# Performance work log

Measured on AMD Instinct MI355X. Metric: run time of the kernel, lower is better.

## Reference

```python
import jax, jax.numpy as jnp
import numpy as np

N, C, H, W = 64, 128, 32, 32
EPS = 1e-5


def _layernorm_chw(x, w, b):
    # LayerNorm over normalized_shape=(C,H,W): last 3 dims
    mu = jnp.mean(x, axis=(1, 2, 3), keepdims=True)
    var = jnp.var(x, axis=(1, 2, 3), keepdims=True)
    return (x - mu) * jax.lax.rsqrt(var + EPS) * w[None] + b[None]


def _conv1x1(x, w, b):
    # x: [N,C,H,W], w: [Cout,Cin], b: [Cout]
    return jnp.einsum('oc,nchw->nohw', w, x) + b[None, :, None, None]


def setup_inputs() -> dict:
    key = jax.random.key(0)
    ks = jax.random.split(key, 12)
    d = {
        'query': jax.random.normal(ks[0], (N, C, H, W), jnp.float32),
        'key': jax.random.normal(ks[1], (N, C, H, W), jnp.float32),
        'value': jax.random.normal(ks[2], (N, C, H, W), jnp.float32),
        'ln1_w': jnp.ones((C, H, W), jnp.float32),
        'ln1_b': jnp.zeros((C, H, W), jnp.float32),
        'ln2_w': jnp.ones((C, H, W), jnp.float32),
        'ln2_b': jnp.zeros((C, H, W), jnp.float32),
        'ln3_w': jnp.ones((C, H, W), jnp.float32),
        'ln3_b': jnp.zeros((C, H, W), jnp.float32),
        'wq': jax.random.normal(ks[3], (C, C), jnp.float32) / np.sqrt(C),
        'bq': jnp.zeros((C,), jnp.float32),
        'wk': jax.random.normal(ks[4], (C, C), jnp.float32) / np.sqrt(C),
        'bk': jnp.zeros((C,), jnp.float32),
        'wv': jax.random.normal(ks[5], (C, C), jnp.float32) / np.sqrt(C),
        'bv': jnp.zeros((C,), jnp.float32),
    }
    return d


def reference(query, key, value, ln1_w, ln1_b, ln2_w, ln2_b, ln3_w, ln3_b,
              wq, bq, wk, bk, wv, bv):
    qn = _layernorm_chw(query, ln1_w, ln1_b)  # residual uses normalized query
    kn = _layernorm_chw(key, ln2_w, ln2_b)
    vn = _layernorm_chw(value, ln3_w, ln3_b)
    q = _conv1x1(qn, wq, bq).reshape(N, C, H * W)
    k = _conv1x1(kn, wk, bk).reshape(N, C, H * W)
    v = _conv1x1(vn, wv, bv).reshape(N, C, H * W)
    # attention[n,i,j] = sum_c k[n,c,i] q[n,c,j] / sqrt(C); softmax over i (dim=1)
    attn = jnp.einsum('nci,ncj->nij', k, q) / jnp.sqrt(jnp.float32(C))
    attn = jax.nn.softmax(attn, axis=1)
    out = jnp.einsum('nci,nij->ncj', v, attn).reshape(N, C, H, W)
    x = qn + out
    return x.reshape(N, -1)  # flatten(start_dim=1)
```

## Files before the change

kernel.cpp:

```cpp
#include <hip/hip_runtime.h>


#define NS 64
#define CD 128
#define SD 1024
#define MEL (CD*SD)
#define SCALE2 0.1275174464f

typedef __attribute__((ext_vector_type(4))) float floatx4;
typedef __attribute__((ext_vector_type(8))) short short8;
typedef __attribute__((ext_vector_type(4))) short short4v;

typedef __attribute__((address_space(1))) const void global_cvoid;
typedef __attribute__((address_space(3))) void lds_void;

__device__ __forceinline__ void gl16(const void* g, void* l) {
  __builtin_amdgcn_global_load_lds((global_cvoid*)g, (lds_void*)l, 16, 0, 0);
}
__device__ __forceinline__ unsigned short f2bf(float f) {
  union { float f; unsigned int i; } v; v.f = f;
  unsigned int i = v.i;
  return (unsigned short)((i + 0x7fffu + ((i >> 16) & 1u)) >> 16);
}
__device__ __forceinline__ unsigned int pkbf(float lo, float hi) {
  unsigned int r;
  asm("v_cvt_pk_bf16_f32 %0, %1, %2" : "=v"(r) : "v"(lo), "v"(hi));
  return r;
}
__device__ __forceinline__ float fexp2(float x) {
  float r; asm("v_exp_f32 %0, %1" : "=v"(r) : "v"(x)); return r;
}
__device__ __forceinline__ short8 ld8_bf16(const float* __restrict__ p) {
  floatx4 a = *(const floatx4*)p;
  floatx4 b = *(const floatx4*)(p + 4);
  union { unsigned int u[4]; short8 s; } r;
  r.u[0] = pkbf(a[0], a[1]);
  r.u[1] = pkbf(a[2], a[3]);
  r.u[2] = pkbf(b[0], b[1]);
  r.u[3] = pkbf(b[2], b[3]);
  return r.s;
}
__device__ __forceinline__ floatx4 mfma16(short8 a, short8 b, floatx4 c) {
  return __builtin_amdgcn_mfma_f32_16x16x32_bf16(a, b, c, 0, 0, 0);
}

__global__ __launch_bounds__(512) void stats_kernel(
    const float* __restrict__ q, const float* __restrict__ k,
    const float* __restrict__ v, float* __restrict__ sums)
{
  int b = blockIdx.x;
  int tn = b >> 2, part = b & 3;
  int t = tn >> 6;
  const float* x = (t == 0 ? q : (t == 1 ? k : v))
                 + (size_t)(tn & 63) * MEL + part * (MEL / 4);
  float s1 = 0.f, s2 = 0.f;
#pragma unroll
  for (int it = 0; it < 16; ++it) {
    floatx4 u = *(const floatx4*)(x + it * 2048 + threadIdx.x * 4);
#pragma unroll
    for (int j = 0; j < 4; ++j) { float f = u[j]; s1 += f; s2 += f * f; }
  }
#pragma unroll
  for (int off = 32; off; off >>= 1) {
    s1 += __shfl_xor(s1, off, 64);
    s2 += __shfl_xor(s2, off, 64);
  }
  __shared__ float r1[8], r2[8];
  int w = threadIdx.x >> 6;
  if ((threadIdx.x & 63) == 0) { r1[w] = s1; r2[w] = s2; }
  __syncthreads();
  if (threadIdx.x == 0) {
    float a = 0.f, c = 0.f;
#pragma unroll
    for (int i = 0; i < 8; ++i) { a += r1[i]; c += r2[i]; }
    sums[part * 192 + tn] = a;
    sums[768 + part * 192 + tn] = c;
  }
}

__device__ __forceinline__ void ln_coeffs(const float* __restrict__ sums,
                                          int g, float& a_ln, float& b_ln)
{
  float s1 = ((sums[g] + sums[192 + g]) + (sums[384 + g] + sums[576 + g]));
  float s2 = ((sums[768 + g] + sums[960 + g]) + (sums[1152 + g] + sums[1344 + g]));
  float mu  = s1 * (1.f / MEL);
  float var = s2 * (1.f / MEL) - mu * mu;
  float rs  = rsqrtf(var + 1e-5f);
  a_ln = rs; b_ln = -mu * rs;
}

__global__ __launch_bounds__(512, 4) void proj_kernel(
  const float* __restrict__ k, const float* __restrict__ v,
  const float* __restrict__ l2w, const float* __restrict__ l2b,
  const float* __restrict__ l3w, const float* __restrict__ l3b,
  const float* __restrict__ wk, const float* __restrict__ bk,
  const float* __restrict__ wv, const float* __restrict__ bv,
  const float* __restrict__ sums,
  unsigned short* __restrict__ kT, unsigned short* __restrict__ vN)
{
  int n  = blockIdx.x, t = blockIdx.y, st = blockIdx.z;
  const float* x  = (t == 0 ? k : v) + (size_t)n * MEL;
  const float* lw = (t == 0 ? l2w : l3w);
  const float* lb = (t == 0 ? l2b : l3b);
  const float* W  = (t == 0 ? wk : wv);
  const float* Bs = (t == 0 ? bk : bv);

  float a_ln, b_ln;
  ln_coeffs(sums, (t + 1) * 64 + n, a_ln, b_ln);

  __shared__ __align__(16) unsigned short Xt[128 * 136];

  int tid = threadIdx.x;
  int cb = tid & 15, sb = (tid >> 4) & 15, half = tid >> 8;
  int s0 = st * 128;

  unsigned int w32[8][2];
#pragma unroll
  for (int pr = 0; pr < 2; ++pr) {
    int c0 = cb * 8 + half * 4 + pr * 2;
    const float* xp0 = x  + (size_t)c0 * SD + s0 + sb * 8;
    const float* wp0 = lw + (size_t)c0 * SD + s0 + sb * 8;
    const float* bp0 = lb + (size_t)c0 * SD + s0 + sb * 8;
    float xv0[8], xv1[8], wv0[8], wv1[8], bv0[8], bv1[8];
    *(floatx4*)xv0 = *(const floatx4*)xp0;       *(floatx4*)(xv0+4) = *(const floatx4*)(xp0+4);
    *(floatx4*)xv1 = *(const floatx4*)(xp0+SD);  *(floatx4*)(xv1+4) = *(const floatx4*)(xp0+SD+4);
    *(floatx4*)wv0 = *(const floatx4*)wp0;       *(floatx4*)(wv0+4) = *(const floatx4*)(wp0+4);
    *(floatx4*)wv1 = *(const floatx4*)(wp0+SD);  *(floatx4*)(wv1+4) = *(const floatx4*)(wp0+SD+4);
    *(floatx4*)bv0 = *(const floatx4*)bp0;       *(floatx4*)(bv0+4) = *(const floatx4*)(bp0+4);
    *(floatx4*)bv1 = *(const floatx4*)(bp0+SD);  *(floatx4*)(bv1+4) = *(const floatx4*)(bp0+SD+4);
#pragma unroll
    for (int js = 0; js < 8; ++js) {
      float lo = (xv0[js] * a_ln + b_ln) * wv0[js] + bv0[js];
      float hi = (xv1[js] * a_ln + b_ln) * wv1[js] + bv1[js];
      w32[js][pr] = pkbf(lo, hi);
    }
  }
#pragma unroll
  for (int js = 0; js < 8; ++js) {
    unsigned int* d = (unsigned int*)&Xt[(sb * 8 + js) * 136 + cb * 8 + half * 4];
    d[0] = w32[js][0]; d[1] = w32[js][1];
  }
  __syncthreads();

  int lane = tid & 63, w = tid >> 6;
  int quad = lane >> 4, l16 = lane & 15;

  short8 Af[4];
#pragma unroll
  for (int kk = 0; kk < 4; ++kk)
    Af[kk] = ld8_bf16(W + (w * 16 + l16) * CD + kk * 32 + quad * 8);

  floatx4 acc[8];
  floatx4 zz = {0.f, 0.f, 0.f, 0.f};
#pragma unroll
  for (int nb = 0; nb < 8; ++nb) acc[nb] = zz;
#pragma unroll
  for (int kk = 0; kk < 4; ++kk)
#pragma unroll
    for (int nb = 0; nb < 8; ++nb) {
      short8 Bf = *(const short8*)&Xt[(nb * 16 + l16) * 136 + kk * 32 + quad * 8];
      acc[nb] = mfma16(Af[kk], Bf, acc[nb]);
    }

  float bsv[4];
#pragma unroll
  for (int r = 0; r < 4; ++r) bsv[r] = Bs[w * 16 + quad * 4 + r];

  __syncthreads();
  unsigned short* Ot = Xt;
#pragma unroll
  for (int nb = 0; nb < 8; ++nb) {
    if (t == 0) {
      unsigned int* d = (unsigned int*)&Ot[(nb * 16 + l16) * 130 + w * 16 + quad * 4];
      d[0] = pkbf(acc[nb][0] + bsv[0], acc[nb][1] + bsv[1]);
      d[1] = pkbf(acc[nb][2] + bsv[2], acc[nb][3] + bsv[3]);
    } else {
      int sl = nb * 16 + l16;
#pragma unroll
      for (int r = 0; r < 4; ++r)
        Ot[(w * 16 + quad * 4 + r) * 130 + sl] = f2bf(acc[nb][r] + bsv[r]);
    }
  }
  __syncthreads();
  unsigned short* gbase = (t == 0) ? (kT + (size_t)n * MEL + (size_t)s0 * CD)
                                   : (vN + (size_t)n * MEL + s0);
#pragma unroll
  for (int p = 0; p < 4; ++p) {
    int g = p * 512 + tid;
    int row = g >> 4, chunk = g & 15;
    short8 val = *(const short8*)&Ot[row * 130 + chunk * 8];
    if (t == 0)
      *(short8*)(gbase + (size_t)row * CD + chunk * 8) = val;
    else
      *(short8*)(gbase + (size_t)row * SD + chunk * 8) = val;
  }
}

__global__ __launch_bounds__(256, 2) void attn_kernel(
  const float* __restrict__ qraw, const float* __restrict__ l1w,
  const float* __restrict__ l1b, const float* __restrict__ wq,
  const float* __restrict__ bq,
  const unsigned short* __restrict__ kT, const unsigned short* __restrict__ vN,
  const float* __restrict__ sums, float* __restrict__ out)
{
  int n = blockIdx.x, jt = blockIdx.y;
  int j0 = jt * 128;

  __shared__ __align__(16) char smem[51712];
  unsigned short* Xt = (unsigned short*)smem;
  unsigned short* Ks = (unsigned short*)smem;
  unsigned short* Vs = (unsigned short*)(smem + 16384);
  unsigned short* Ps = (unsigned short*)(smem + 34816);
  float* l_s = (float*)(smem + 51200);

  int tid = threadIdx.x, lane = tid & 63, w = tid >> 6;
  int quad = lane >> 4, l16 = lane & 15;

  float a_ln, b_ln;
  ln_coeffs(sums, n, a_ln, b_ln);
  const float* qb = qraw + (size_t)n * MEL;

  {
    int cb = tid & 15, sb = tid >> 4;
    unsigned int w32[8][4];
#pragma unroll
    for (int pr = 0; pr < 4; ++pr) {
      int c0 = cb * 8 + pr * 2;
      const float* xp0 = qb  + (size_t)c0 * SD + j0 + sb * 8;
      const float* wp0 = l1w + (size_t)c0 * SD + j0 + sb * 8;
      const float* bp0 = l1b + (size_t)c0 * SD + j0 + sb * 8;
      float xv0[8], xv1[8], wv0[8], wv1[8], bv0[8], bv1[8];
      *(floatx4*)xv0 = *(const floatx4*)xp0;       *(floatx4*)(xv0+4) = *(const floatx4*)(xp0+4);
      *(floatx4*)xv1 = *(const floatx4*)(xp0+SD);  *(floatx4*)(xv1+4) = *(const floatx4*)(xp0+SD+4);
      *(floatx4*)wv0 = *(const floatx4*)wp0;       *(floatx4*)(wv0+4) = *(const floatx4*)(wp0+4);
      *(floatx4*)wv1 = *(const floatx4*)(wp0+SD);  *(floatx4*)(wv1+4) = *(const floatx4*)(wp0+SD+4);
      *(floatx4*)bv0 = *(const floatx4*)bp0;       *(floatx4*)(bv0+4) = *(const floatx4*)(bp0+4);
      *(floatx4*)bv1 = *(const floatx4*)(bp0+SD);  *(floatx4*)(bv1+4) = *(const floatx4*)(bp0+SD+4);
#pragma unroll
      for (int js = 0; js < 8; ++js) {
        float lo = (xv0[js] * a_ln + b_ln) * wv0[js] + bv0[js];
        float hi = (xv1[js] * a_ln + b_ln) * wv1[js] + bv1[js];
        w32[js][pr] = pkbf(lo, hi);
      }
    }
#pragma unroll
    for (int js = 0; js < 8; ++js)
      *(floatx4*)&Xt[(sb * 8 + js) * 136 + cb * 8] = *(floatx4*)w32[js];
  }
  __syncthreads();

  floatx4 zz = {0.f, 0.f, 0.f, 0.f};
  {
    short8 Af[2][4];
#pragma unroll
    for (int mi = 0; mi < 2; ++mi)
#pragma unroll
      for (int kk = 0; kk < 4; ++kk)
        Af[mi][kk] = ld8_bf16(wq + ((w * 2 + mi) * 16 + l16) * CD + kk * 32 + quad * 8);
    floatx4 accq[2][8];
#pragma unroll
    for (int mi = 0; mi < 2; ++mi)
#pragma unroll
      for (int nb = 0; nb < 8; ++nb) accq[mi][nb] = zz;
#pragma unroll
    for (int kk = 0; kk < 4; ++kk)
#pragma unroll
      for (int nb = 0; nb < 8; ++nb) {
        short8 Bf = *(const short8*)&Xt[(nb * 16 + l16) * 136 + kk * 32 + quad * 8];
        accq[0][nb] = mfma16(Af[0][kk], Bf, accq[0][nb]);
        accq[1][nb] = mfma16(Af[1][kk], Bf, accq[1][nb]);
      }
    __syncthreads();
    float bqs[2][4];
#pragma unroll
    for (int mi = 0; mi < 2; ++mi)
#pragma unroll
      for (int r = 0; r < 4; ++r) bqs[mi][r] = bq[(w * 2 + mi) * 16 + quad * 4 + r];
#pragma unroll
    for (int mi = 0; mi < 2; ++mi)
#pragma unroll
      for (int nb = 0; nb < 8; ++nb) {
        unsigned int* d = (unsigned int*)&Xt[(nb * 16 + l16) * 136 + (w * 2 + mi) * 16 + quad * 4];
        d[0] = pkbf(accq[mi][nb][0] + bqs[mi][0], accq[mi][nb][1] + bqs[mi][1]);
        d[1] = pkbf(accq[mi][nb][2] + bqs[mi][2], accq[mi][nb][3] + bqs[mi][3]);
      }
  }
  __syncthreads();

  short8 Qf[2][4];
#pragma unroll
  for (int nt = 0; nt < 2; ++nt)
#pragma unroll
    for (int kk = 0; kk < 4; ++kk)
      Qf[nt][kk] = *(const short8*)&Xt[((w * 2 + nt) * 16 + l16) * 136 + kk * 32 + quad * 8];
  __syncthreads();

  floatx4 Oc[2][8];
#pragma unroll
  for (int mi = 0; mi < 2; ++mi)
#pragma unroll
    for (int nb = 0; nb < 8; ++nb) Oc[mi][nb] = zz;
  float lsum[2] = {0.f, 0.f};

  const unsigned short* kbase0 = kT + (size_t)n * MEL;
  const unsigned short* vbase0 = vN + (size_t)n * MEL;

  for (int itile = 0; itile < 16; ++itile) {
    int i0 = itile * 64;
    const unsigned short* kbase = kbase0 + (size_t)i0 * CD;
#pragma unroll
    for (int it = 0; it < 4; ++it) {
      int nch = w * 256 + it * 64 + lane;
      int i = nch >> 4, cc = nch & 15;
      int csrc = (cc & 8) | ((cc & 7) ^ (i & 7));
      gl16(kbase + i * CD + csrc * 8, (char*)Ks + (w * 256 + it * 64) * 16);
    }
#pragma unroll
    for (int it = 0; it < 4; ++it) {
      int nch = w * 256 + it * 64 + lane;
      int c = nch >> 3, ci = nch & 7;
      int isrc = ci ^ (c & 7);
      gl16(vbase0 + (size_t)c * SD + i0 + isrc * 8, (char*)Vs + (w * 256 + it * 64) * 16);
    }
    __syncthreads();

    floatx4 Sa[4][2];
#pragma unroll
    for (int mt = 0; mt < 4; ++mt) { Sa[mt][0] = zz; Sa[mt][1] = zz; }
    __builtin_amdgcn_s_setprio(1);
#pragma unroll
    for (int kk = 0; kk < 4; ++kk)
#pragma unroll
      for (int mt = 0; mt < 4; ++mt) {
        short8 Kf = *(const short8*)&Ks[(mt * 16 + l16) * 128 + (((kk * 4 + quad) ^ (l16 & 7)) * 8)];
        Sa[mt][0] = mfma16(Kf, Qf[0][kk], Sa[mt][0]);
        Sa[mt][1] = mfma16(Kf, Qf[1][kk], Sa[mt][1]);
      }
    __builtin_amdgcn_s_setprio(0);

#pragma unroll
    for (int nt = 0; nt < 2; ++nt) {
      int jrow = (w * 2 + nt) * 16 + l16;
      int rowbase = jrow * 64;
      int sub = (quad & 1) * 4;
#pragma unroll
      for (int mt = 0; mt < 4; ++mt) {
        float p0 = fexp2(Sa[mt][nt][0] * SCALE2);
        float p1 = fexp2(Sa[mt][nt][1] * SCALE2);
        float p2 = fexp2(Sa[mt][nt][2] * SCALE2);
        float p3 = fexp2(Sa[mt][nt][3] * SCALE2);
        lsum[nt] += (p0 + p1) + (p2 + p3);
        int ci = mt * 2 + (quad >> 1);
        int cis = ci ^ (l16 & 7);
        unsigned int* d = (unsigned int*)&Ps[rowbase + cis * 8 + sub];
        d[0] = pkbf(p0, p1);
        d[1] = pkbf(p2, p3);
      }
    }
    __syncthreads();

#pragma unroll
    for (int kk = 0; kk < 2; ++kk) {
      short8 Vf[2];
#pragma unroll
      for (int mi = 0; mi < 2; ++mi) {
        int c = (w * 2 + mi) * 16 + l16;
        Vf[mi] = *(const short8*)&Vs[c * 64 + (((kk * 4 + quad) ^ (l16 & 7)) * 8)];
      }
      __builtin_amdgcn_s_setprio(1);
#pragma unroll
      for (int nb = 0; nb < 8; ++nb) {
        short8 Pf = *(const short8*)&Ps[(nb * 16 + l16) * 64 + (((kk * 4 + quad) ^ (l16 & 7)) * 8)];
        Oc[0][nb] = mfma16(Vf[0], Pf, Oc[0][nb]);
        Oc[1][nb] = mfma16(Vf[1], Pf, Oc[1][nb]);
      }
      __builtin_amdgcn_s_setprio(0);
    }
    __syncthreads();
  }

#pragma unroll
  for (int nt = 0; nt < 2; ++nt) {
    lsum[nt] += __shfl_xor(lsum[nt], 16, 64);
    lsum[nt] += __shfl_xor(lsum[nt], 32, 64);
  }
  if (lane < 16) { l_s[(w * 2) * 16 + l16] = lsum[0]; l_s[(w * 2 + 1) * 16 + l16] = lsum[1]; }
  __syncthreads();

  float linv[8];
#pragma unroll
  for (int nb = 0; nb < 8; ++nb) linv[nb] = 1.f / l_s[nb * 16 + l16];
#pragma unroll
  for (int mi = 0; mi < 2; ++mi) {
#pragma unroll
    for (int r = 0; r < 4; ++r) {
      int c = (w * 2 + mi) * 16 + quad * 4 + r;
      const float* qp = qb  + (size_t)c * SD + j0;
      const float* wp = l1w + (size_t)c * SD + j0;
      const float* bp = l1b + (size_t)c * SD + j0;
      float* op = out + (size_t)n * MEL + (size_t)c * SD + j0;
#pragma unroll
      for (int nb = 0; nb < 8; ++nb) {
        int j = nb * 16 + l16;
        float qn = (qp[j] * a_ln + b_ln) * wp[j] + bp[j];
        op[j] = Oc[mi][nb][r] * linv[nb] + qn;
      }
    }
  }
}

extern "C" void kernel_launch(void* const* d_in, const int* in_sizes, int n_in,
                              void* d_out, int out_size, void* d_ws, size_t ws_size,
                              hipStream_t stream)
{
  const float* q   = (const float*)d_in[0];
  const float* k   = (const float*)d_in[1];
  const float* v   = (const float*)d_in[2];
  const float* l1w = (const float*)d_in[3];
  const float* l1b = (const float*)d_in[4];
  const float* l2w = (const float*)d_in[5];
  const float* l2b = (const float*)d_in[6];
  const float* l3w = (const float*)d_in[7];
  const float* l3b = (const float*)d_in[8];
  const float* wq  = (const float*)d_in[9];
  const float* bq  = (const float*)d_in[10];
  const float* wk  = (const float*)d_in[11];
  const float* bk  = (const float*)d_in[12];
  const float* wv  = (const float*)d_in[13];
  const float* bv  = (const float*)d_in[14];

  char* ws = (char*)d_ws;
  float* sums = (float*)ws;
  unsigned short* kT = (unsigned short*)(ws + 8192);
  unsigned short* vN = kT + (size_t)NS * MEL;

  stats_kernel<<<768, 512, 0, stream>>>(q, k, v, sums);
  proj_kernel<<<dim3(64, 2, 8), 512, 0, stream>>>(k, v, l2w, l2b, l3w, l3b,
      wk, bk, wv, bv, sums, kT, vN);
  attn_kernel<<<dim3(64, 8), 256, 0, stream>>>(q, l1w, l1b, wq, bq, kT, vN,
      sums, (float*)d_out);
}
```

Baseline: 249.4 us.

## Halve attention query tile to 64 columns and double grid blocks

The attention kernel now handles 64 query positions per block instead of 128. The grid doubles to 64x16 blocks, and shared memory and accumulator registers shrink, so occupancy can rise to three blocks per CU. This is meant to fill the 256 CUs better, since the old 512-block grid underused the GPU. The cost is that each K/V tile is loaded from global memory twice as many times in total, and each block does less MFMA work per load.

```diff
diff --git a/kernel.cpp b/kernel.cpp
--- a/kernel.cpp
+++ b/kernel.cpp
@@ -196,7 +196,7 @@
   }
 }
 
-__global__ __launch_bounds__(256, 2) void attn_kernel(
+__global__ __launch_bounds__(256, 3) void attn_kernel(
   const float* __restrict__ qraw, const float* __restrict__ l1w,
   const float* __restrict__ l1b, const float* __restrict__ wq,
   const float* __restrict__ bq,
@@ -204,14 +204,14 @@
   const float* __restrict__ sums, float* __restrict__ out)
 {
   int n = blockIdx.x, jt = blockIdx.y;
-  int j0 = jt * 128;
-
-  __shared__ __align__(16) char smem[51712];
+  int j0 = jt * 64;
+
+  __shared__ __align__(16) char smem[41216];
   unsigned short* Xt = (unsigned short*)smem;
   unsigned short* Ks = (unsigned short*)smem;
   unsigned short* Vs = (unsigned short*)(smem + 16384);
-  unsigned short* Ps = (unsigned short*)(smem + 34816);
-  float* l_s = (float*)(smem + 51200);
+  unsigned short* Ps = (unsigned short*)(smem + 32768);
+  float* l_s = (float*)(smem + 40960);
 
   int tid = threadIdx.x, lane = tid & 63, w = tid >> 6;
   int quad = lane >> 4, l16 = lane & 15;
@@ -221,11 +221,11 @@
   const float* qb = qraw + (size_t)n * MEL;
 
   {
-    int cb = tid & 15, sb = tid >> 4;
-    unsigned int w32[8][4];
-#pragma unroll
-    for (int pr = 0; pr < 4; ++pr) {
-      int c0 = cb * 8 + pr * 2;
+    int cb = tid & 15, sb = (tid >> 4) & 7, half = tid >> 7;
+    unsigned int w32[8][2];
+#pragma unroll
+    for (int pr = 0; pr < 2; ++pr) {
+      int c0 = cb * 8 + half * 4 + pr * 2;
       const float* xp0 = qb  + (size_t)c0 * SD + j0 + sb * 8;
       const float* wp0 = l1w + (size_t)c0 * SD + j0 + sb * 8;
       const float* bp0 = l1b + (size_t)c0 * SD + j0 + sb * 8;
@@ -244,8 +244,10 @@
       }
     }
 #pragma unroll
-    for (int js = 0; js < 8; ++js)
-      *(floatx4*)&Xt[(sb * 8 + js) * 136 + cb * 8] = *(floatx4*)w32[js];
+    for (int js = 0; js < 8; ++js) {
+      unsigned int* d = (unsigned int*)&Xt[(sb * 8 + js) * 136 + cb * 8 + half * 4];
+      d[0] = w32[js][0]; d[1] = w32[js][1];
+    }
   }
   __syncthreads();
 
@@ -257,15 +259,15 @@
 #pragma unroll
       for (int kk = 0; kk < 4; ++kk)
         Af[mi][kk] = ld8_bf16(wq + ((w * 2 + mi) * 16 + l16) * CD + kk * 32 + quad * 8);
-    floatx4 accq[2][8];
+    floatx4 accq[2][4];
 #pragma unroll
     for (int mi = 0; mi < 2; ++mi)
 #pragma unroll
-      for (int nb = 0; nb < 8; ++nb) accq[mi][nb] = zz;
+      for (int nb = 0; nb < 4; ++nb) accq[mi][nb] = zz;
 #pragma unroll
     for (int kk = 0; kk < 4; ++kk)
 #pragma unroll
-      for (int nb = 0; nb < 8; ++nb) {
+      for (int nb = 0; nb < 4; ++nb) {
         short8 Bf = *(const short8*)&Xt[(nb * 16 + l16) * 136 + kk * 32 + quad * 8];
         accq[0][nb] = mfma16(Af[0][kk], Bf, accq[0][nb]);
         accq[1][nb] = mfma16(Af[1][kk], Bf, accq[1][nb]);
@@ -279,7 +281,7 @@
 #pragma unroll
     for (int mi = 0; mi < 2; ++mi)
 #pragma unroll
-      for (int nb = 0; nb < 8; ++nb) {
+      for (int nb = 0; nb < 4; ++nb) {
         unsigned int* d = (unsigned int*)&Xt[(nb * 16 + l16) * 136 + (w * 2 + mi) * 16 + quad * 4];
         d[0] = pkbf(accq[mi][nb][0] + bqs[mi][0], accq[mi][nb][1] + bqs[mi][1]);
         d[1] = pkbf(accq[mi][nb][2] + bqs[mi][2], accq[mi][nb][3] + bqs[mi][3]);
@@ -287,20 +289,18 @@
   }
   __syncthreads();
 
-  short8 Qf[2][4];
-#pragma unroll
-  for (int nt = 0; nt < 2; ++nt)
-#pragma unroll
-    for (int kk = 0; kk < 4; ++kk)
-      Qf[nt][kk] = *(const short8*)&Xt[((w * 2 + nt) * 16 + l16) * 136 + kk * 32 + quad * 8];
-  __syncthreads();
-
-  floatx4 Oc[2][8];
+  short8 Qf[4];
+#pragma unroll
+  for (int kk = 0; kk < 4; ++kk)
+    Qf[kk] = *(const short8*)&Xt[(w * 16 + l16) * 136 + kk * 32 + quad * 8];
+  __syncthreads();
+
+  floatx4 Oc[2][4];
 #pragma unroll
   for (int mi = 0; mi < 2; ++mi)
 #pragma unroll
-    for (int nb = 0; nb < 8; ++nb) Oc[mi][nb] = zz;
-  float lsum[2] = {0.f, 0.f};
+    for (int nb = 0; nb < 4; ++nb) Oc[mi][nb] = zz;
+  float lsum = 0.f;
 
   const unsigned short* kbase0 = kT + (size_t)n * MEL;
   const unsigned short* vbase0 = vN + (size_t)n * MEL;
@@ -324,32 +324,30 @@
     }
     __syncthreads();
 
-    floatx4 Sa[4][2];
-#pragma unroll
-    for (int mt = 0; mt < 4; ++mt) { Sa[mt][0] = zz; Sa[mt][1] = zz; }
+    floatx4 Sa[4];
+#pragma unroll
+    for (int mt = 0; mt < 4; ++mt) Sa[mt] = zz;
     __builtin_amdgcn_s_setprio(1);
 #pragma unroll
     for (int kk = 0; kk < 4; ++kk)
 #pragma unroll
       for (int mt = 0; mt < 4; ++mt) {
         short8 Kf = *(const short8*)&Ks[(mt * 16 + l16) * 128 + (((kk * 4 + quad) ^ (l16 & 7)) * 8)];
-        Sa[mt][0] = mfma16(Kf, Qf[0][kk], Sa[mt][0]);
-        Sa[mt][1] = mfma16(Kf, Qf[1][kk], Sa[mt][1]);
+        Sa[mt] = mfma16(Kf, Qf[kk], Sa[mt]);
       }
     __builtin_amdgcn_s_setprio(0);
 
-#pragma unroll
-    for (int nt = 0; nt < 2; ++nt) {
-      int jrow = (w * 2 + nt) * 16 + l16;
+    {
+      int jrow = w * 16 + l16;
       int rowbase = jrow * 64;
       int sub = (quad & 1) * 4;
 #pragma unroll
       for (int mt = 0; mt < 4; ++mt) {
-        float p0 = fexp2(Sa[mt][nt][0] * SCALE2);
-        float p1 = fexp2(Sa[mt][nt][1] * SCALE2);
-        float p2 = fexp2(Sa[mt][nt][2] * SCALE2);
-        float p3 = fexp2(Sa[mt][nt][3] * SCALE2);
-        lsum[nt] += (p0 + p1) + (p2 + p3);
+        float p0 = fexp2(Sa[mt][0] * SCALE2);
+        float p1 = fexp2(Sa[mt][1] * SCALE2);
+        float p2 = fexp2(Sa[mt][2] * SCALE2);
+        float p3 = fexp2(Sa[mt][3] * SCALE2);
+        lsum += (p0 + p1) + (p2 + p3);
         int ci = mt * 2 + (quad >> 1);
         int cis = ci ^ (l16 & 7);
         unsigned int* d = (unsigned int*)&Ps[rowbase + cis * 8 + sub];
@@ -369,7 +367,7 @@
       }
       __builtin_amdgcn_s_setprio(1);
 #pragma unroll
-      for (int nb = 0; nb < 8; ++nb) {
+      for (int nb = 0; nb < 4; ++nb) {
         short8 Pf = *(const short8*)&Ps[(nb * 16 + l16) * 64 + (((kk * 4 + quad) ^ (l16 & 7)) * 8)];
         Oc[0][nb] = mfma16(Vf[0], Pf, Oc[0][nb]);
         Oc[1][nb] = mfma16(Vf[1], Pf, Oc[1][nb]);
@@ -379,17 +377,14 @@
     __syncthreads();
   }
 
-#pragma unroll
-  for (int nt = 0; nt < 2; ++nt) {
-    lsum[nt] += __shfl_xor(lsum[nt], 16, 64);
-    lsum[nt] += __shfl_xor(lsum[nt], 32, 64);
-  }
-  if (lane < 16) { l_s[(w * 2) * 16 + l16] = lsum[0]; l_s[(w * 2 + 1) * 16 + l16] = lsum[1]; }
-  __syncthreads();
-
-  float linv[8];
-#pragma unroll
-  for (int nb = 0; nb < 8; ++nb) linv[nb] = 1.f / l_s[nb * 16 + l16];
+  lsum += __shfl_xor(lsum, 16, 64);
+  lsum += __shfl_xor(lsum, 32, 64);
+  if (lane < 16) l_s[w * 16 + l16] = lsum;
+  __syncthreads();
+
+  float linv[4];
+#pragma unroll
+  for (int nb = 0; nb < 4; ++nb) linv[nb] = 1.f / l_s[nb * 16 + l16];
 #pragma unroll
   for (int mi = 0; mi < 2; ++mi) {
 #pragma unroll
@@ -400,7 +395,7 @@
       const float* bp = l1b + (size_t)c * SD + j0;
       float* op = out + (size_t)n * MEL + (size_t)c * SD + j0;
 #pragma unroll
-      for (int nb = 0; nb < 8; ++nb) {
+      for (int nb = 0; nb < 4; ++nb) {
         int j = nb * 16 + l16;
         float qn = (qp[j] * a_ln + b_ln) * wp[j] + bp[j];
         op[j] = Oc[mi][nb][r] * linv[nb] + qn;
@@ -437,6 +432,6 @@
   stats_kernel<<<768, 512, 0, stream>>>(q, k, v, sums);
   proj_kernel<<<dim3(64, 2, 8), 512, 0, stream>>>(k, v, l2w, l2b, l3w, l3b,
       wk, bk, wv, bv, sums, kT, vN);
-  attn_kernel<<<dim3(64, 8), 256, 0, stream>>>(q, l1w, l1b, wq, bq, kT, vN,
+  attn_kernel<<<dim3(64, 16), 256, 0, stream>>>(q, l1w, l1b, wq, bq, kT, vN,
       sums, (float*)d_out);
 }
```

New measurement: 261.5 us. 4.8% more time.

## Double-buffer K/V tiles in LDS and prefetch next tile during compute

Applied to the files above, without the earlier changes.

Shared memory now holds two K/V tile buffers. The next tile's global-to-LDS loads are issued before computing on the current one, with explicit vmcnt waits and raw barriers in place of __syncthreads. The first tile is prefetched at kernel entry so it overlaps with the query LayerNorm and projection prologue. This aims to hide global load latency behind MFMA work, but LDS grows from about 51KB to 80KB, which may reduce occupancy below the requested 2 blocks per CU.

```diff
diff --git a/kernel.cpp b/kernel.cpp
--- a/kernel.cpp
+++ b/kernel.cpp
@@ -196,6 +196,30 @@
   }
 }
 
+__device__ __forceinline__ void stage_tile(
+    const unsigned short* __restrict__ kbase0,
+    const unsigned short* __restrict__ vbase0,
+    char* smem, int ti, int buf, int w, int lane)
+{
+  const unsigned short* kb = kbase0 + (size_t)ti * 64 * CD;
+  char* KD = smem + buf * 32768;
+  char* VD = smem + buf * 32768 + 16384;
+#pragma unroll
+  for (int it = 0; it < 4; ++it) {
+    int nch = w * 256 + it * 64 + lane;
+    int i = nch >> 4, cc = nch & 15;
+    int csrc = (cc & 8) | ((cc & 7) ^ (i & 7));
+    gl16(kb + i * CD + csrc * 8, KD + (w * 256 + it * 64) * 16);
+  }
+#pragma unroll
+  for (int it = 0; it < 4; ++it) {
+    int nch = w * 256 + it * 64 + lane;
+    int c = nch >> 3, ci = nch & 7;
+    int isrc = ci ^ (c & 7);
+    gl16(vbase0 + (size_t)c * SD + ti * 64 + isrc * 8, VD + (w * 256 + it * 64) * 16);
+  }
+}
+
 __global__ __launch_bounds__(256, 2) void attn_kernel(
   const float* __restrict__ qraw, const float* __restrict__ l1w,
   const float* __restrict__ l1b, const float* __restrict__ wq,
@@ -206,15 +230,18 @@
   int n = blockIdx.x, jt = blockIdx.y;
   int j0 = jt * 128;
 
-  __shared__ __align__(16) char smem[51712];
-  unsigned short* Xt = (unsigned short*)smem;
-  unsigned short* Ks = (unsigned short*)smem;
-  unsigned short* Vs = (unsigned short*)(smem + 16384);
-  unsigned short* Ps = (unsigned short*)(smem + 34816);
-  float* l_s = (float*)(smem + 51200);
+  __shared__ __align__(16) char smem[81920];
+  unsigned short* Xt = (unsigned short*)(smem + 32768);
+  unsigned short* Ps = (unsigned short*)(smem + 65536);
+  float* l_s = (float*)smem;
 
   int tid = threadIdx.x, lane = tid & 63, w = tid >> 6;
   int quad = lane >> 4, l16 = lane & 15;
+
+  const unsigned short* kbase0 = kT + (size_t)n * MEL;
+  const unsigned short* vbase0 = vN + (size_t)n * MEL;
+
+  stage_tile(kbase0, vbase0, smem, 0, 0, w, lane);
 
   float a_ln, b_ln;
   ln_coeffs(sums, n, a_ln, b_ln);
@@ -302,27 +329,19 @@
     for (int nb = 0; nb < 8; ++nb) Oc[mi][nb] = zz;
   float lsum[2] = {0.f, 0.f};
 
-  const unsigned short* kbase0 = kT + (size_t)n * MEL;
-  const unsigned short* vbase0 = vN + (size_t)n * MEL;
-
   for (int itile = 0; itile < 16; ++itile) {
-    int i0 = itile * 64;
-    const unsigned short* kbase = kbase0 + (size_t)i0 * CD;
-#pragma unroll
-    for (int it = 0; it < 4; ++it) {
-      int nch = w * 256 + it * 64 + lane;
-      int i = nch >> 4, cc = nch & 15;
-      int csrc = (cc & 8) | ((cc & 7) ^ (i & 7));
-      gl16(kbase + i * CD + csrc * 8, (char*)Ks + (w * 256 + it * 64) * 16);
-    }
-#pragma unroll
-    for (int it = 0; it < 4; ++it) {
-      int nch = w * 256 + it * 64 + lane;
-      int c = nch >> 3, ci = nch & 7;
-      int isrc = ci ^ (c & 7);
-      gl16(vbase0 + (size_t)c * SD + i0 + isrc * 8, (char*)Vs + (w * 256 + it * 64) * 16);
-    }
-    __syncthreads();
+    int buf = itile & 1;
+    if (itile < 15) {
+      stage_tile(kbase0, vbase0, smem, itile + 1, buf ^ 1, w, lane);
+      asm volatile("s_waitcnt vmcnt(8)" ::: "memory");
+    } else {
+      asm volatile("s_waitcnt vmcnt(0)" ::: "memory");
+    }
+    __builtin_amdgcn_s_barrier();
+    __builtin_amdgcn_sched_barrier(0);
+
+    const unsigned short* Ks = (const unsigned short*)(smem + buf * 32768);
+    const unsigned short* Vs = (const unsigned short*)(smem + buf * 32768 + 16384);
 
     floatx4 Sa[4][2];
 #pragma unroll
@@ -357,7 +376,9 @@
         d[1] = pkbf(p2, p3);
       }
     }
-    __syncthreads();
+    asm volatile("s_waitcnt lgkmcnt(0)" ::: "memory");
+    __builtin_amdgcn_s_barrier();
+    __builtin_amdgcn_sched_barrier(0);
 
 #pragma unroll
     for (int kk = 0; kk < 2; ++kk) {
@@ -376,7 +397,9 @@
       }
       __builtin_amdgcn_s_setprio(0);
     }
-    __syncthreads();
+    asm volatile("s_waitcnt lgkmcnt(0)" ::: "memory");
+    __builtin_amdgcn_s_barrier();
+    __builtin_amdgcn_sched_barrier(0);
   }
 
 #pragma unroll
```

Measured after the change: 249.0 us. About the same (-0.2%).
